# Kernel tuning notes

Hardware: AMD Instinct MI355X
Metric: run time of the kernel (lower is better)

Reference implementation:

```python
import jax, jax.numpy as jnp
import numpy as np

B, T, HID = 2, 2048, 3840
H, KV, D = 16, 8, 256
EPS = 1e-6
WINDOW = 1024
THETA_LOCAL = 10000.0
THETA_GLOBAL = 1000000.0


def _rope_tables(theta, t, d):
    inv_freq = 1.0 / (theta ** (jnp.arange(0, d, 2, dtype=jnp.float32) / d))  # (d/2,)
    ang = jnp.arange(t, dtype=jnp.float32)[:, None] * inv_freq[None, :]        # (T, d/2)
    return jnp.cos(ang), jnp.sin(ang)


def setup_inputs() -> dict:
    key = jax.random.key(0)
    ks = jax.random.split(key, 8)
    x = jax.random.normal(ks[0], (B, T, HID), dtype=jnp.float32)
    wq = jax.random.normal(ks[1], (H * D, HID), dtype=jnp.float32) * 0.02
    wk = jax.random.normal(ks[2], (KV * D, HID), dtype=jnp.float32) * 0.02
    wv = jax.random.normal(ks[3], (KV * D, HID), dtype=jnp.float32) * 0.02
    wo = jax.random.normal(ks[4], (HID, H * D), dtype=jnp.float32) * 0.02
    q_norm_w = 1.0 + jax.random.normal(ks[5], (D,), dtype=jnp.float32) * 0.02
    k_norm_w = 1.0 + jax.random.normal(ks[6], (D,), dtype=jnp.float32) * 0.02
    cos_g, sin_g = _rope_tables(THETA_GLOBAL, T, D)
    cos_l, sin_l = _rope_tables(THETA_LOCAL, T, D)
    # causal + sliding-window(1024) additive float mask, shape (1,1,T,T)
    i = jnp.arange(T)[:, None]
    j = jnp.arange(T)[None, :]
    allowed = (j <= i) & (i - j < WINDOW)
    attention_mask = jnp.where(allowed, 0.0, -1e9).astype(jnp.float32)[None, None]
    return {"x": x, "cos_global": cos_g, "sin_global": sin_g, "cos_local": cos_l,
            "sin_local": sin_l, "attention_mask": attention_mask,
            "wq": wq, "wk": wk, "wv": wv, "wo": wo,
            "q_norm_w": q_norm_w, "k_norm_w": k_norm_w}


def _rms_norm(x, w):
    # add=False variant: x * rsqrt(mean(x^2)+eps) * w, computed in fp32
    norm = jax.lax.rsqrt(jnp.mean(jnp.square(x), axis=-1, keepdims=True) + EPS)
    return x * norm * w


def _apply_rope(x, cos, sin):
    # x: (B, H, T, D); cos/sin: (T, D/2)
    t = x.shape[2]
    c = cos[:t][None, None]
    s = sin[:t][None, None]
    x1, x2 = x[..., : x.shape[-1] // 2], x[..., x.shape[-1] // 2 :]
    return jnp.concatenate([x1 * c - x2 * s, x2 * c + x1 * s], axis=-1)


def reference(x, cos_global, sin_global, cos_local, sin_local, attention_mask,
              wq, wk, wv, wo, q_norm_w, k_norm_w):
    b, t, _ = x.shape
    q = (x @ wq.T).reshape(b, t, H, D).transpose(0, 2, 1, 3)   # (B,H,T,D)
    k = (x @ wk.T).reshape(b, t, KV, D).transpose(0, 2, 1, 3)  # (B,KV,T,D)
    v = (x @ wv.T).reshape(b, t, KV, D).transpose(0, 2, 1, 3)
    q = _rms_norm(q, q_norm_w)
    k = _rms_norm(k, k_norm_w)
    # layer_idx=0 -> sliding-window layer -> local rope
    q = _apply_rope(q, cos_local, sin_local)
    k = _apply_rope(k, cos_local, sin_local)
    rep = H // KV
    k = jnp.repeat(k, rep, axis=1)  # repeat_interleave over head dim
    v = jnp.repeat(v, rep, axis=1)
    scale = 1.0 / jnp.sqrt(jnp.float32(D))
    scores = jnp.einsum("bhqd,bhkd->bhqk", q, k) * scale + attention_mask
    attn = jax.nn.softmax(scores, axis=-1)
    out = jnp.einsum("bhqk,bhkd->bhqd", attn, v)
    out = out.transpose(0, 2, 1, 3).reshape(b, t, H * D)
    return out @ wo.T
```

## Files before the change

kernel.cpp:

```cpp
#include <hip/hip_runtime.h>
#include <hip/hip_bf16.h>

typedef __hip_bfloat16 BF;
typedef __attribute__((ext_vector_type(8))) short short8;
typedef __attribute__((ext_vector_type(4))) float f32x4;

#define DEV __device__ __forceinline__

DEV void gll16(const BF* g, BF* l) {
  __builtin_amdgcn_global_load_lds(
      (const __attribute__((address_space(1))) void*)g,
      (__attribute__((address_space(3))) void*)l, 16, 0, 0);
}

DEV unsigned short bfbits(float f) {
  BF b = __float2bfloat16(f);
  return *reinterpret_cast<unsigned short*>(&b);
}

DEV ushort4 cvt4(const float4 v) {
  return make_ushort4(bfbits(v.x), bfbits(v.y), bfbits(v.z), bfbits(v.w));
}

DEV int rope_perm(int d) {
  return (d < 128) ? ((d >> 5) * 64 + (d & 31))
                   : (((d - 128) >> 5) * 64 + 32 + ((d - 128) & 31));
}

__global__ void cvt_fused(const float* __restrict__ x, const float* __restrict__ wq,
                          const float* __restrict__ wk, const float* __restrict__ wv,
                          const float* __restrict__ wo,
                          BF* __restrict__ Xbf, BF* __restrict__ Wqkv, BF* __restrict__ Wo) {
  const int stride = gridDim.x * blockDim.x;
  for (int i = blockIdx.x * blockDim.x + threadIdx.x; i < 15728640; i += stride) {
    if (i < 3932160) {
      ((ushort4*)Xbf)[i] = cvt4(((const float4*)x)[i]);
    } else if (i < 7864320) {
      const int off = i - 3932160;
      const int row = off / 960, col = off - row * 960;
      const int nrow = (row & ~255) | rope_perm(row & 255);
      ((ushort4*)Wqkv)[nrow * 960 + col] = cvt4(((const float4*)wq)[off]);
    } else if (i < 9830400) {
      const int off = i - 7864320;
      const int row = off / 960, col = off - row * 960;
      const int nrow = (row & ~255) | rope_perm(row & 255);
      ((ushort4*)(Wqkv + 4096 * 3840))[nrow * 960 + col] = cvt4(((const float4*)wk)[off]);
    } else if (i < 11796480) {
      const int off = i - 9830400;
      ((ushort4*)(Wqkv + 6144 * 3840))[off] = cvt4(((const float4*)wv)[off]);
    } else {
      const int off = i - 11796480;
      const int r = off >> 10, c = off & 1023;
      ((ushort4*)Wo)[r * 1040 + c] = cvt4(((const float4*)wo)[off]);
    }
  }
}

#define PHASE(MH, KK, READB, STAGE, TAIL)                                            \
  {                                                                                  \
    short8 af[4];                                                                    \
    const BF* Ap = Ax + (KK)*8192;                                                   \
    _Pragma("unroll") for (int m = 0; m < 4; ++m)                                    \
        af[m] = *(const short8*)&Ap[(wm*128 + (MH)*64 + m*16 + l15) * 32 + rd8];     \
    if (READB) {                                                                     \
      const BF* Bp = Bx + (KK)*8192;                                                 \
      _Pragma("unroll") for (int n = 0; n < 4; ++n)                                  \
          breg[n] = *(const short8*)&Bp[(wn*64 + n*16 + l15) * 32 + rd8];            \
    }                                                                                \
    STAGE                                                                            \
    __builtin_amdgcn_s_barrier();                                                    \
    asm volatile("s_waitcnt lgkmcnt(0)" ::: "memory");                               \
    __builtin_amdgcn_sched_barrier(0);                                               \
    __builtin_amdgcn_s_setprio(1);                                                   \
    _Pragma("unroll") for (int m = 0; m < 4; ++m)                                    \
      _Pragma("unroll") for (int n = 0; n < 4; ++n)                                  \
        acc[(MH)*4 + m][n] =                                                         \
            __builtin_amdgcn_mfma_f32_16x16x32_bf16(af[m], breg[n], acc[(MH)*4+m][n], 0, 0, 0); \
    __builtin_amdgcn_s_setprio(0);                                                   \
    TAIL                                                                             \
    __builtin_amdgcn_s_barrier();                                                    \
  }

#define STG2(SRC, RST, DST) { gll16((SRC), (DST)); gll16((SRC) + (RST), (DST) + 4096); }

template <typename CT, int MODE>
DEV void gemm256_body(const BF* __restrict__ A, const BF* __restrict__ Bm,
                      CT* __restrict__ C, const int M, const int N, const int K,
                      const int lda, const int ldb,
                      BF* __restrict__ Qb, BF* __restrict__ Kb,
                      const float* __restrict__ cosl, const float* __restrict__ sinl,
                      const float* __restrict__ qw, const float* __restrict__ kw) {
  extern __shared__ __align__(16) BF lds[];
  BF* ldsA = lds;
  BF* ldsB = lds + 32768;
  const int ntl = N >> 8;
  const int mtl = M >> 8;
  int mt, nt;
  if (mtl == 16 && ntl == 32) {
    const int x = blockIdx.x & 7;
    const int c = blockIdx.x >> 3;
    mt = ((x >> 2) << 3) + (c >> 3);
    nt = ((x & 3) << 3) + (c & 7);
  } else {
    const int cpx = gridDim.x >> 3;
    const int swzb = (blockIdx.x & 7) * cpx + (blockIdx.x >> 3);
    mt = swzb / ntl;
    nt = swzb % ntl;
  }
  const int m0 = mt << 8, n0 = nt << 8;
  const int tid = threadIdx.x, lane = tid & 63, w = tid >> 6;
  const int l15 = lane & 15, g = lane >> 4;
  const int wm = w >> 2, wn = w & 3;
  const int rd8 = (g ^ ((l15 >> 1) & 3)) << 3;
  const int trow = tid >> 2;
  const int scol = ((lane & 3) ^ ((lane >> 3) & 3)) << 3;
  const BF* aS = A + (size_t)(m0 + trow) * lda + scol;
  const BF* bS = Bm + (size_t)(n0 + trow) * ldb + scol;
  const size_t rstpA = (size_t)128 * lda;
  const size_t rstpB = (size_t)128 * ldb;
  BF* dA = ldsA + w * 512;
  BF* dB = ldsB + w * 512;
  const int NT = K >> 6;

  f32x4 acc[8][4];
#pragma unroll
  for (int m = 0; m < 8; ++m)
#pragma unroll
    for (int n = 0; n < 4; ++n) acc[m][n] = (f32x4){0.f, 0.f, 0.f, 0.f};
  short8 breg[4];

  STG2(aS, rstpA, dA);
  STG2(bS, rstpB, dB);
  STG2(aS + 32, rstpA, dA + 8192);
  STG2(bS + 32, rstpB, dB + 8192);
  STG2(aS + 64, rstpA, dA + 16384);
  STG2(bS + 64, rstpB, dB + 16384);
  asm volatile("s_waitcnt vmcnt(8)" ::: "memory");
  __builtin_amdgcn_sched_barrier(0);
  __builtin_amdgcn_s_barrier();

  for (int t = 0; t < NT; ++t) {
    const int bX = (t & 1) << 14;
    const int bY = bX ^ 16384;
    const BF* Ax = ldsA + bX;
    const BF* Bx = ldsB + bX;
    const int kc1 = (t + 1) << 6, kc2 = (t + 2) << 6;
    const bool s1 = (t + 1 < NT), s2 = (t + 2 < NT);
    PHASE(0, 0, 1, if (s1) STG2(aS + kc1 + 32, rstpA, dA + bY + 8192);, )
    PHASE(1, 0, 0, if (s1) STG2(bS + kc1 + 32, rstpB, dB + bY + 8192);,
          { asm volatile("s_waitcnt vmcnt(8)" ::: "memory");
            __builtin_amdgcn_sched_barrier(0); } )
    PHASE(0, 1, 1, if (s2) STG2(aS + kc2, rstpA, dA + bX);, )
    PHASE(1, 1, 0, if (s2) STG2(bS + kc2, rstpB, dB + bX);,
          if (s2) { asm volatile("s_waitcnt vmcnt(8)" ::: "memory");
                    __builtin_amdgcn_sched_barrier(0); }
          else    { asm volatile("s_waitcnt vmcnt(0)" ::: "memory");
                    __builtin_amdgcn_sched_barrier(0); } )
  }

  if constexpr (MODE == 0) {
#pragma unroll
    for (int mi = 0; mi < 8; ++mi) {
      const int gr = m0 + wm * 128 + mi * 16 + g * 4;
#pragma unroll
      for (int n = 0; n < 4; ++n) {
        const int gc = n0 + wn * 64 + n * 16 + l15;
#pragma unroll
        for (int r = 0; r < 4; ++r)
          C[(size_t)(gr + r) * N + gc] = acc[mi][n][r];
      }
    }
  } else {
    if (nt >= 24) {
#pragma unroll
      for (int mi = 0; mi < 8; ++mi) {
        const int gr = m0 + wm * 128 + mi * 16 + g * 4;
#pragma unroll
        for (int n = 0; n < 4; ++n) {
          const int gc = n0 - 6144 + wn * 64 + n * 16 + l15;
#pragma unroll
          for (int r = 0; r < 4; ++r)
            C[(size_t)(gr + r) * 2048 + gc] = __float2bfloat16(acc[mi][n][r]);
        }
      }
    } else {
      const bool isq = (nt < 16);
      const int head = isq ? nt : (nt - 16);
      const float* wgt = isq ? qw : kw;
      float* red = (float*)lds;
      __builtin_amdgcn_s_barrier();
#pragma unroll
      for (int mi = 0; mi < 8; ++mi) {
        float ps[4];
#pragma unroll
        for (int r = 0; r < 4; ++r) {
          float s = 0.f;
#pragma unroll
          for (int n = 0; n < 4; ++n) s += acc[mi][n][r] * acc[mi][n][r];
#pragma unroll
          for (int mm = 1; mm < 16; mm <<= 1) s += __shfl_xor(s, mm);
          ps[r] = s;
        }
        if (l15 == 0) {
          const int rb = wm * 128 + mi * 16 + g * 4;
#pragma unroll
          for (int r = 0; r < 4; ++r) red[(rb + r) * 4 + wn] = ps[r];
        }
      }
      __syncthreads();
      float rms[8][4];
#pragma unroll
      for (int mi = 0; mi < 8; ++mi)
#pragma unroll
        for (int r = 0; r < 4; ++r) {
          const int row = wm * 128 + mi * 16 + g * 4 + r;
          const float4 p = *(const float4*)&red[row * 4];
          rms[mi][r] = rsqrtf((p.x + p.y + p.z + p.w) * (1.f / 256.f) + 1e-6f);
        }
#pragma unroll
      for (int mi = 0; mi < 8; ++mi) {
#pragma unroll
        for (int r = 0; r < 4; ++r) {
          const int grow = m0 + wm * 128 + mi * 16 + g * 4 + r;
          const int tt = grow & 2047, bb = grow >> 11;
          const float rm = rms[mi][r];
          BF* orow = (isq ? Qb + ((size_t)(bb * 16 + head) * 2048 + tt) * 256
                          : Kb + ((size_t)(bb * 8 + head) * 2048 + tt) * 256);
#pragma unroll
          for (int n = 0; n < 2; ++n) {
            const int dlo = wn * 32 + n * 16 + l15;
            const float cc = cosl[tt * 128 + dlo];
            const float ss = sinl[tt * 128 + dlo];
            const float xl = acc[mi][n][r] * rm * wgt[dlo];
            const float xh = acc[mi][n + 2][r] * rm * wgt[dlo + 128];
            const int cbase = wn * 64 + n * 16 + l15;
            orow[cbase]      = __float2bfloat16(xl * cc - xh * ss);
            orow[cbase + 32] = __float2bfloat16(xh * cc + xl * ss);
          }
        }
      }
    }
  }
}

__global__ __launch_bounds__(512, 2) void gemm_qkv(const BF* __restrict__ A,
                                                   const BF* __restrict__ Bm,
                                                   BF* __restrict__ C1v,
                                                   BF* __restrict__ Qb, BF* __restrict__ Kb,
                                                   const float* __restrict__ cosl,
                                                   const float* __restrict__ sinl,
                                                   const float* __restrict__ qw,
                                                   const float* __restrict__ kw,
                                                   int M, int N, int K, int lda, int ldb) {
  gemm256_body<BF, 1>(A, Bm, C1v, M, N, K, lda, ldb, Qb, Kb, cosl, sinl, qw, kw);
}
__global__ __launch_bounds__(512, 2) void gemm_out(const BF* __restrict__ A,
                                                   const BF* __restrict__ Bm,
                                                   float* __restrict__ C,
                                                   int M, int N, int K, int lda, int ldb) {
  gemm256_body<float, 0>(A, Bm, C, M, N, K, lda, ldb,
                         nullptr, nullptr, nullptr, nullptr, nullptr, nullptr);
}

__global__ __launch_bounds__(256) void vtrans(const BF* __restrict__ C1v, BF* __restrict__ Vt) {
  __shared__ BF tile[64][68];
  const int bz = blockIdx.z;
  const int tt = blockIdx.x;
  const int dt = blockIdx.y;
  const int tid = threadIdx.x;
  const int r16 = tid >> 4;
  const int c16 = tid & 15;
  const int b = bz >> 3, kv = bz & 7;
#pragma unroll
  for (int p = 0; p < 4; ++p) {
    const int tr = p * 16 + r16;
    const int t = tt * 64 + tr;
    const int d = dt * 64 + c16 * 4;
    *(ushort4*)&tile[tr][c16 * 4] =
        *(const ushort4*)&C1v[((size_t)(b * 2048 + t)) * 2048 + kv * 256 + d];
  }
  __syncthreads();
#pragma unroll
  for (int p = 0; p < 4; ++p) {
    const int dr = p * 16 + r16;
    const int d = dt * 64 + dr;
    const int t4 = c16 * 4;
    ushort4 o;
    o.x = *(const unsigned short*)&tile[t4 + 0][dr];
    o.y = *(const unsigned short*)&tile[t4 + 1][dr];
    o.z = *(const unsigned short*)&tile[t4 + 2][dr];
    o.w = *(const unsigned short*)&tile[t4 + 3][dr];
    *(ushort4*)&Vt[((size_t)bz * 256 + d) * 2048 + tt * 64 + t4] = o;
  }
}

__global__ __launch_bounds__(512, 1) void attn_fwd(const BF* __restrict__ Q,
                                                   const BF* __restrict__ K,
                                                   const BF* __restrict__ Vt,
                                                   BF* __restrict__ O) {
  __shared__ __align__(16) BF Ks[64 * 256];
  __shared__ __align__(16) BF Vs[256 * 64];
  __shared__ __align__(16) BF Ps[8][1024];
  const int tid = threadIdx.x;
  const int lane = tid & 63;
  const int w = tid >> 6;
  const int wh = w >> 2;
  const int wq = w & 3;
  const int l15 = lane & 15;
  const int g = lane >> 4;
  const int qt = blockIdx.x;
  const int bp = blockIdx.y;
  const int b = bp >> 3, kvh = bp & 7;
  const int h = kvh * 2 + wh;
  const int q0 = qt << 6;
  const BF* Qb = Q + ((size_t)(b * 16 + h) * 2048 + q0) * 256;
  const BF* Kb = K + (size_t)(b * 8 + kvh) * 2048 * 256;
  const BF* Vb = Vt + (size_t)(b * 8 + kvh) * 256 * 2048;

  short8 qf[8];
  {
    const BF* qr = Qb + (wq * 16 + l15) * 256 + g * 8;
#pragma unroll
    for (int kk = 0; kk < 8; ++kk) qf[kk] = *(const short8*)(qr + kk * 32);
  }
  f32x4 oacc[16];
#pragma unroll
  for (int i = 0; i < 16; ++i) oacc[i] = (f32x4){0.f, 0.f, 0.f, 0.f};
  float m_r[4] = {-1e30f, -1e30f, -1e30f, -1e30f};
  float l_r[4] = {0.f, 0.f, 0.f, 0.f};

  const int kt_lo = (q0 > 1023) ? ((q0 - 1023) >> 6) : 0;
  for (int kt = kt_lo; kt <= qt; ++kt) {
    const int tk = kt << 6;
#pragma unroll
    for (int i = 0; i < 4; ++i) {
      const int li = w * 4 + i;
      {
        const int row = li * 2 + (lane >> 5);
        const int ch = lane & 31;
        gll16(Kb + (size_t)(tk + row) * 256 + ((ch ^ (row & 7)) << 3), Ks + li * 512);
      }
      {
        const int row = li * 8 + (lane >> 3);
        const int ch = lane & 7;
        gll16(Vb + (size_t)row * 2048 + tk + ((ch ^ (row & 7)) << 3), Vs + li * 512);
      }
    }
    __syncthreads();

    f32x4 sa[4];
#pragma unroll
    for (int i2 = 0; i2 < 4; ++i2) sa[i2] = (f32x4){0.f, 0.f, 0.f, 0.f};
#pragma unroll
    for (int kk = 0; kk < 8; ++kk) {
      const int d = kk * 32 + g * 8;
#pragma unroll
      for (int blk = 0; blk < 4; ++blk) {
        const int row = blk * 16 + l15;
        const short8 kf = *(const short8*)&Ks[row * 256 + (d ^ ((row & 7) << 3))];
        sa[blk] = __builtin_amdgcn_mfma_f32_16x16x32_bf16(qf[kk], kf, sa[blk], 0, 0, 0);
      }
    }

    float al4[4];
#pragma unroll
    for (int r = 0; r < 4; ++r) {
      const int qi = q0 + wq * 16 + g * 4 + r;
      float pv[4];
      float tmax = -1e30f;
#pragma unroll
      for (int blk = 0; blk < 4; ++blk) {
        const int ki = tk + blk * 16 + l15;
        float sv = sa[blk][r] * 0.0625f;
        const bool ok = (ki <= qi) && (qi - ki < 1024);
        sv = ok ? sv : -1e30f;
        pv[blk] = sv;
        tmax = fmaxf(tmax, sv);
      }
#pragma unroll
      for (int mm = 1; mm < 16; mm <<= 1) tmax = fmaxf(tmax, __shfl_xor(tmax, mm));
      const float mn = fmaxf(m_r[r], tmax);
      const float alpha = __expf(m_r[r] - mn);
      float tsum = 0.f;
#pragma unroll
      for (int blk = 0; blk < 4; ++blk) {
        const float p = __expf(pv[blk] - mn);
        pv[blk] = p;
        tsum += p;
      }
#pragma unroll
      for (int mm = 1; mm < 16; mm <<= 1) tsum += __shfl_xor(tsum, mm);
      l_r[r] = l_r[r] * alpha + tsum;
      m_r[r] = mn;
      al4[r] = alpha;
      const int prow = g * 4 + r;
#pragma unroll
      for (int blk = 0; blk < 4; ++blk) {
        const int col = blk * 16 + l15;
        Ps[w][prow * 64 + (col ^ ((prow & 7) << 3))] = __float2bfloat16(pv[blk]);
      }
    }
#pragma unroll
    for (int db = 0; db < 16; ++db)
#pragma unroll
      for (int r = 0; r < 4; ++r) oacc[db][r] *= al4[r];

#pragma unroll
    for (int kk2 = 0; kk2 < 2; ++kk2) {
      const int k8 = kk2 * 32 + g * 8;
      const short8 pf = *(const short8*)&Ps[w][l15 * 64 + (k8 ^ ((l15 & 7) << 3))];
#pragma unroll
      for (int db = 0; db < 16; ++db) {
        const int vrow = db * 16 + l15;
        const short8 vf = *(const short8*)&Vs[vrow * 64 + (k8 ^ ((vrow & 7) << 3))];
        oacc[db] = __builtin_amdgcn_mfma_f32_16x16x32_bf16(pf, vf, oacc[db], 0, 0, 0);
      }
    }
    __syncthreads();
  }

#pragma unroll
  for (int r = 0; r < 4; ++r) l_r[r] = 1.f / l_r[r];
  const size_t orow0 = (size_t)(b * 2048 + q0 + wq * 16 + g * 4);
#pragma unroll
  for (int r = 0; r < 4; ++r) {
    BF* op = O + (orow0 + r) * 4160 + h * 256 + l15;
#pragma unroll
    for (int db = 0; db < 16; ++db) op[db * 16] = __float2bfloat16(oacc[db][r] * l_r[r]);
  }
}

extern "C" void kernel_launch(void* const* d_in, const int* in_sizes, int n_in,
                              void* d_out, int out_size, void* d_ws, size_t ws_size,
                              hipStream_t stream) {
  (void)in_sizes; (void)n_in; (void)out_size;
  const float* x    = (const float*)d_in[0];
  const float* cosl = (const float*)d_in[3];
  const float* sinl = (const float*)d_in[4];
  const float* wq   = (const float*)d_in[6];
  const float* wk   = (const float*)d_in[7];
  const float* wv   = (const float*)d_in[8];
  const float* wo   = (const float*)d_in[9];
  const float* qw   = (const float*)d_in[10];
  const float* kw   = (const float*)d_in[11];
  float* out = (float*)d_out;
  char* ws = (char*)d_ws;
  if (ws_size < 193429504ull) return;

  BF* Wqkv = (BF*)(ws + 0);
  BF* Xbf  = (BF*)(ws + 62914560);
  BF* Qb   = (BF*)(ws + 94371840);
  BF* Kb   = (BF*)(ws + 127926272);
  BF* C1v  = (BF*)(ws + 144703488);
  BF* Wo   = (BF*)(ws + 161480704);
  BF* Vt   = (BF*)(ws + 0);
  BF* AO   = (BF*)(ws + 16777216);

  hipFuncSetAttribute(reinterpret_cast<const void*>(gemm_qkv),
                      hipFuncAttributeMaxDynamicSharedMemorySize, 131072);
  hipFuncSetAttribute(reinterpret_cast<const void*>(gemm_out),
                      hipFuncAttributeMaxDynamicSharedMemorySize, 131072);

  cvt_fused<<<2048, 256, 0, stream>>>(x, wq, wk, wv, wo, Xbf, Wqkv, Wo);

  gemm_qkv<<<512, 512, 131072, stream>>>(Xbf, Wqkv, C1v, Qb, Kb, cosl, sinl, qw, kw,
                                         4096, 8192, 3840, 3840, 3840);
  vtrans<<<dim3(32, 4, 16), 256, 0, stream>>>(C1v, Vt);
  attn_fwd<<<dim3(32, 16), 512, 0, stream>>>(Qb, Kb, Vt, AO);
  gemm_out<<<240, 512, 131072, stream>>>(AO, Wo, out, 4096, 3840, 4096, 4160, 4160);
}
```

Baseline: 568.0 us.

## Use 4-wave 256x256 GEMM tiles with 128x128 per-wave subtiles

Both GEMMs now launch 256 threads instead of 512, so each of the 4 waves owns a 128x128 output subtile (an 8x8 MFMA accumulator grid) rather than 128x64. Global-to-LDS staging is restructured so each thread issues four loads per half-tile, and the RMS-norm reduction and RoPE epilogue indexing are adapted to two column-waves. The aim is more MFMA work per LDS fragment read, cutting LDS traffic per flop. In exchange each wave roughly doubles its accumulator registers, and fewer waves per block means less latency hiding.

```diff
diff --git a/kernel.cpp b/kernel.cpp
--- a/kernel.cpp
+++ b/kernel.cpp
@@ -56,32 +56,40 @@
   }
 }
 
-#define PHASE(MH, KK, READB, STAGE, TAIL)                                            \
-  {                                                                                  \
-    short8 af[4];                                                                    \
-    const BF* Ap = Ax + (KK)*8192;                                                   \
-    _Pragma("unroll") for (int m = 0; m < 4; ++m)                                    \
-        af[m] = *(const short8*)&Ap[(wm*128 + (MH)*64 + m*16 + l15) * 32 + rd8];     \
-    if (READB) {                                                                     \
-      const BF* Bp = Bx + (KK)*8192;                                                 \
-      _Pragma("unroll") for (int n = 0; n < 4; ++n)                                  \
-          breg[n] = *(const short8*)&Bp[(wn*64 + n*16 + l15) * 32 + rd8];            \
-    }                                                                                \
-    STAGE                                                                            \
-    __builtin_amdgcn_s_barrier();                                                    \
-    asm volatile("s_waitcnt lgkmcnt(0)" ::: "memory");                               \
-    __builtin_amdgcn_sched_barrier(0);                                               \
-    __builtin_amdgcn_s_setprio(1);                                                   \
-    _Pragma("unroll") for (int m = 0; m < 4; ++m)                                    \
-      _Pragma("unroll") for (int n = 0; n < 4; ++n)                                  \
-        acc[(MH)*4 + m][n] =                                                         \
-            __builtin_amdgcn_mfma_f32_16x16x32_bf16(af[m], breg[n], acc[(MH)*4+m][n], 0, 0, 0); \
-    __builtin_amdgcn_s_setprio(0);                                                   \
-    TAIL                                                                             \
-    __builtin_amdgcn_s_barrier();                                                    \
-  }
-
-#define STG2(SRC, RST, DST) { gll16((SRC), (DST)); gll16((SRC) + (RST), (DST) + 4096); }
+#define WAITV(N)                                                                      \
+  asm volatile("s_waitcnt vmcnt(" #N ")" ::: "memory");                               \
+  __builtin_amdgcn_sched_barrier(0);
+#define STGA(KC, BOFF)                                                                \
+  _Pragma("unroll") for (int j_ = 0; j_ < 4; ++j_)                                    \
+      gll16(aS + (size_t)(j_ * 64) * lda + (KC), ldsA + (BOFF) + j_ * 2048 + w * 512);
+#define STGB(KC, BOFF)                                                                \
+  _Pragma("unroll") for (int j_ = 0; j_ < 4; ++j_)                                    \
+      gll16(bS + (size_t)(j_ * 64) * ldb + (KC), ldsB + (BOFF) + j_ * 2048 + w * 512);
+#define GPHASE(MH, KK, READB, STAGE, TAIL)                                            \
+  {                                                                                   \
+    short8 af[4];                                                                     \
+    _Pragma("unroll") for (int m_ = 0; m_ < 4; ++m_)                                  \
+        af[m_] = *(const short8*)&ldsA[bX + (KK)*8192 +                               \
+                                       (wm*128 + (MH)*64 + m_*16 + l15)*32 + rd8];    \
+    if (READB) {                                                                      \
+      _Pragma("unroll") for (int n_ = 0; n_ < 8; ++n_)                                \
+          breg[n_] = *(const short8*)&ldsB[bX + (KK)*8192 +                           \
+                                           (wn*128 + n_*16 + l15)*32 + rd8];          \
+    }                                                                                 \
+    STAGE                                                                             \
+    __builtin_amdgcn_s_barrier();                                                     \
+    asm volatile("s_waitcnt lgkmcnt(0)" ::: "memory");                                \
+    __builtin_amdgcn_sched_barrier(0);                                                \
+    __builtin_amdgcn_s_setprio(1);                                                    \
+    _Pragma("unroll") for (int m_ = 0; m_ < 4; ++m_)                                  \
+      _Pragma("unroll") for (int n_ = 0; n_ < 8; ++n_)                                \
+        acc[(MH)*4 + m_][n_] =                                                        \
+            __builtin_amdgcn_mfma_f32_16x16x32_bf16(af[m_], breg[n_],                 \
+                                                    acc[(MH)*4 + m_][n_], 0, 0, 0);   \
+    __builtin_amdgcn_s_setprio(0);                                                    \
+    TAIL                                                                              \
+    __builtin_amdgcn_s_barrier();                                                     \
+  }
 
 template <typename CT, int MODE>
 DEV void gemm256_body(const BF* __restrict__ A, const BF* __restrict__ Bm,
@@ -110,52 +118,37 @@
   const int m0 = mt << 8, n0 = nt << 8;
   const int tid = threadIdx.x, lane = tid & 63, w = tid >> 6;
   const int l15 = lane & 15, g = lane >> 4;
-  const int wm = w >> 2, wn = w & 3;
+  const int wm = w >> 1, wn = w & 1;
   const int rd8 = (g ^ ((l15 >> 1) & 3)) << 3;
-  const int trow = tid >> 2;
-  const int scol = ((lane & 3) ^ ((lane >> 3) & 3)) << 3;
-  const BF* aS = A + (size_t)(m0 + trow) * lda + scol;
-  const BF* bS = Bm + (size_t)(n0 + trow) * ldb + scol;
-  const size_t rstpA = (size_t)128 * lda;
-  const size_t rstpB = (size_t)128 * ldb;
-  BF* dA = ldsA + w * 512;
-  BF* dB = ldsB + w * 512;
+  const int scol = ((tid & 3) ^ ((tid >> 3) & 3)) << 3;
+  const BF* aS = A + (size_t)(m0 + (tid >> 2)) * lda + scol;
+  const BF* bS = Bm + (size_t)(n0 + (tid >> 2)) * ldb + scol;
   const int NT = K >> 6;
 
-  f32x4 acc[8][4];
+  f32x4 acc[8][8];
 #pragma unroll
   for (int m = 0; m < 8; ++m)
 #pragma unroll
-    for (int n = 0; n < 4; ++n) acc[m][n] = (f32x4){0.f, 0.f, 0.f, 0.f};
-  short8 breg[4];
-
-  STG2(aS, rstpA, dA);
-  STG2(bS, rstpB, dB);
-  STG2(aS + 32, rstpA, dA + 8192);
-  STG2(bS + 32, rstpB, dB + 8192);
-  STG2(aS + 64, rstpA, dA + 16384);
-  STG2(bS + 64, rstpB, dB + 16384);
-  asm volatile("s_waitcnt vmcnt(8)" ::: "memory");
-  __builtin_amdgcn_sched_barrier(0);
+    for (int n = 0; n < 8; ++n) acc[m][n] = (f32x4){0.f, 0.f, 0.f, 0.f};
+  short8 breg[8];
+
+  STGA(0, 0) STGB(0, 0)
+  STGA(32, 8192) STGB(32, 8192)
+  STGA(64, 16384) STGB(64, 16384)
+  WAITV(8)
   __builtin_amdgcn_s_barrier();
 
   for (int t = 0; t < NT; ++t) {
     const int bX = (t & 1) << 14;
     const int bY = bX ^ 16384;
-    const BF* Ax = ldsA + bX;
-    const BF* Bx = ldsB + bX;
     const int kc1 = (t + 1) << 6, kc2 = (t + 2) << 6;
     const bool s1 = (t + 1 < NT), s2 = (t + 2 < NT);
-    PHASE(0, 0, 1, if (s1) STG2(aS + kc1 + 32, rstpA, dA + bY + 8192);, )
-    PHASE(1, 0, 0, if (s1) STG2(bS + kc1 + 32, rstpB, dB + bY + 8192);,
-          { asm volatile("s_waitcnt vmcnt(8)" ::: "memory");
-            __builtin_amdgcn_sched_barrier(0); } )
-    PHASE(0, 1, 1, if (s2) STG2(aS + kc2, rstpA, dA + bX);, )
-    PHASE(1, 1, 0, if (s2) STG2(bS + kc2, rstpB, dB + bX);,
-          if (s2) { asm volatile("s_waitcnt vmcnt(8)" ::: "memory");
-                    __builtin_amdgcn_sched_barrier(0); }
-          else    { asm volatile("s_waitcnt vmcnt(0)" ::: "memory");
-                    __builtin_amdgcn_sched_barrier(0); } )
+    GPHASE(0, 0, 1, if (s1) STGA(kc1 + 32, bY + 8192), )
+    GPHASE(1, 0, 0, if (s1) STGB(kc1 + 32, bY + 8192),
+           if (s1) { WAITV(8) } else { WAITV(0) })
+    GPHASE(0, 1, 1, if (s2) STGA(kc2, bX), )
+    GPHASE(1, 1, 0, if (s2) STGB(kc2, bX),
+           if (s2) { WAITV(8) } else { WAITV(0) })
   }
 
   if constexpr (MODE == 0) {
@@ -163,8 +156,8 @@
     for (int mi = 0; mi < 8; ++mi) {
       const int gr = m0 + wm * 128 + mi * 16 + g * 4;
 #pragma unroll
-      for (int n = 0; n < 4; ++n) {
-        const int gc = n0 + wn * 64 + n * 16 + l15;
+      for (int n = 0; n < 8; ++n) {
+        const int gc = n0 + wn * 128 + n * 16 + l15;
 #pragma unroll
         for (int r = 0; r < 4; ++r)
           C[(size_t)(gr + r) * N + gc] = acc[mi][n][r];
@@ -176,8 +169,8 @@
       for (int mi = 0; mi < 8; ++mi) {
         const int gr = m0 + wm * 128 + mi * 16 + g * 4;
 #pragma unroll
-        for (int n = 0; n < 4; ++n) {
-          const int gc = n0 - 6144 + wn * 64 + n * 16 + l15;
+        for (int n = 0; n < 8; ++n) {
+          const int gc = n0 - 6144 + wn * 128 + n * 16 + l15;
 #pragma unroll
           for (int r = 0; r < 4; ++r)
             C[(size_t)(gr + r) * 2048 + gc] = __float2bfloat16(acc[mi][n][r]);
@@ -196,7 +189,7 @@
         for (int r = 0; r < 4; ++r) {
           float s = 0.f;
 #pragma unroll
-          for (int n = 0; n < 4; ++n) s += acc[mi][n][r] * acc[mi][n][r];
+          for (int n = 0; n < 8; ++n) s += acc[mi][n][r] * acc[mi][n][r];
 #pragma unroll
           for (int mm = 1; mm < 16; mm <<= 1) s += __shfl_xor(s, mm);
           ps[r] = s;
@@ -204,7 +197,7 @@
         if (l15 == 0) {
           const int rb = wm * 128 + mi * 16 + g * 4;
 #pragma unroll
-          for (int r = 0; r < 4; ++r) red[(rb + r) * 4 + wn] = ps[r];
+          for (int r = 0; r < 4; ++r) red[(rb + r) * 2 + wn] = ps[r];
         }
       }
       __syncthreads();
@@ -214,8 +207,8 @@
 #pragma unroll
         for (int r = 0; r < 4; ++r) {
           const int row = wm * 128 + mi * 16 + g * 4 + r;
-          const float4 p = *(const float4*)&red[row * 4];
-          rms[mi][r] = rsqrtf((p.x + p.y + p.z + p.w) * (1.f / 256.f) + 1e-6f);
+          const float2 p = *(const float2*)&red[row * 2];
+          rms[mi][r] = rsqrtf((p.x + p.y) * (1.f / 256.f) + 1e-6f);
         }
 #pragma unroll
       for (int mi = 0; mi < 8; ++mi) {
@@ -227,13 +220,14 @@
           BF* orow = (isq ? Qb + ((size_t)(bb * 16 + head) * 2048 + tt) * 256
                           : Kb + ((size_t)(bb * 8 + head) * 2048 + tt) * 256);
 #pragma unroll
-          for (int n = 0; n < 2; ++n) {
-            const int dlo = wn * 32 + n * 16 + l15;
+          for (int nn = 0; nn < 4; ++nn) {
+            const int n = (nn & 1) | ((nn & 2) << 1);
+            const int dlo = (wn * 2 + (n >> 2)) * 32 + (n & 1) * 16 + l15;
             const float cc = cosl[tt * 128 + dlo];
             const float ss = sinl[tt * 128 + dlo];
             const float xl = acc[mi][n][r] * rm * wgt[dlo];
             const float xh = acc[mi][n + 2][r] * rm * wgt[dlo + 128];
-            const int cbase = wn * 64 + n * 16 + l15;
+            const int cbase = wn * 128 + n * 16 + l15;
             orow[cbase]      = __float2bfloat16(xl * cc - xh * ss);
             orow[cbase + 32] = __float2bfloat16(xh * cc + xl * ss);
           }
@@ -243,7 +237,7 @@
   }
 }
 
-__global__ __launch_bounds__(512, 2) void gemm_qkv(const BF* __restrict__ A,
+__global__ __launch_bounds__(256, 1) void gemm_qkv(const BF* __restrict__ A,
                                                    const BF* __restrict__ Bm,
                                                    BF* __restrict__ C1v,
                                                    BF* __restrict__ Qb, BF* __restrict__ Kb,
@@ -254,7 +248,7 @@
                                                    int M, int N, int K, int lda, int ldb) {
   gemm256_body<BF, 1>(A, Bm, C1v, M, N, K, lda, ldb, Qb, Kb, cosl, sinl, qw, kw);
 }
-__global__ __launch_bounds__(512, 2) void gemm_out(const BF* __restrict__ A,
+__global__ __launch_bounds__(256, 1) void gemm_out(const BF* __restrict__ A,
                                                    const BF* __restrict__ Bm,
                                                    float* __restrict__ C,
                                                    int M, int N, int K, int lda, int ldb) {
@@ -463,9 +457,9 @@
 
   cvt_fused<<<2048, 256, 0, stream>>>(x, wq, wk, wv, wo, Xbf, Wqkv, Wo);
 
-  gemm_qkv<<<512, 512, 131072, stream>>>(Xbf, Wqkv, C1v, Qb, Kb, cosl, sinl, qw, kw,
+  gemm_qkv<<<512, 256, 131072, stream>>>(Xbf, Wqkv, C1v, Qb, Kb, cosl, sinl, qw, kw,
                                          4096, 8192, 3840, 3840, 3840);
   vtrans<<<dim3(32, 4, 16), 256, 0, stream>>>(C1v, Vt);
   attn_fwd<<<dim3(32, 16), 512, 0, stream>>>(Qb, Kb, Vt, AO);
-  gemm_out<<<240, 512, 131072, stream>>>(AO, Wo, out, 4096, 3840, 4096, 4160, 4160);
-}
+  gemm_out<<<240, 256, 131072, stream>>>(AO, Wo, out, 4096, 3840, 4096, 4160, 4160);
+}
```

After: 671.1 us. 18.1% more time.
